# Performance work log

Hardware: AMD Instinct MI355X
Metric: run time of the kernel (lower is better)

Reference implementation:

```python
import jax, jax.numpy as jnp
import numpy as np

N, D, M, E, K = 16384, 512, 1024, 8, 2
LOSS_COEF = 0.01
EPS = 1e-10


def setup_inputs() -> dict:
    key = jax.random.key(0)
    ks = jax.random.split(key, 6)
    x = jax.random.normal(ks[0], (N, D), dtype=jnp.float32)
    # gate weight (torch init is zeros; use small random so routing is non-degenerate)
    w_gate = 0.02 * jax.random.normal(ks[1], (D, E), dtype=jnp.float32)
    # stacked expert FFN params: Linear(D->M), GELU, Linear(M->D)
    W1 = jax.random.normal(ks[2], (E, D, M), dtype=jnp.float32) / np.sqrt(D)
    b1 = jnp.zeros((E, M), dtype=jnp.float32)
    W2 = jax.random.normal(ks[3], (E, M, D), dtype=jnp.float32) / np.sqrt(M)
    b2 = jnp.zeros((E, D), dtype=jnp.float32)
    return {"x": x, "w_gate": w_gate, "W1": W1, "b1": b1, "W2": W2, "b2": b2}


def _cv_squared(v):
    # torch .var() is unbiased (ddof=1)
    v = v.astype(jnp.float32)
    return jnp.var(v, ddof=1) / (jnp.mean(v) ** 2 + EPS)


def reference(x, w_gate, W1, b1, W2, b2):
    n = x.shape[0]
    # --- noisy_top_k_gating (eval path: no noise) ---
    logits = x @ w_gate                                  # [N, E]
    top_logits, top_idx = jax.lax.top_k(logits, min(K + 1, E))
    topk_logits = top_logits[:, :K]                      # [N, K]
    topk_idx = top_idx[:, :K]                            # [N, K]
    topk_gates = jax.nn.softmax(topk_logits, axis=-1)    # [N, K]
    gates = jnp.zeros_like(logits).at[jnp.arange(n)[:, None], topk_idx].set(topk_gates)
    importance = gates.sum(axis=0)                       # [E]
    load = (gates > 0).sum(axis=0).astype(jnp.float32)   # [E]
    loss = LOSS_COEF * (_cv_squared(importance) + _cv_squared(load))
    # --- experts (dense equivalent of sparse dispatch/combine: gate==0 rows contribute 0) ---
    h = jnp.einsum('nd,edm->enm', x, W1) + b1[:, None, :]     # [E, N, M]
    h = jax.nn.gelu(h, approximate=False)
    out = jnp.einsum('enm,emd->end', h, W2) + b2[:, None, :]  # [E, N, D]
    y = jnp.einsum('ne,end->nd', gates, out)                  # [N, D]
    return (y, loss)
```

## Files before the change

### kernel.cpp

```cpp
#include <hip/hip_runtime.h>
#include <math.h>

#define NTOK 16384
#define DDIM 512
#define MDIM 1024
#define NEXP 8
#define BKW 32
#define TMAX 264

typedef __attribute__((ext_vector_type(8))) short short8;
typedef __attribute__((ext_vector_type(4))) float floatx4;

__device__ inline unsigned short f2bf(float f){
  union { float f; unsigned int u; } v; v.f = f;
  unsigned int u = v.u;
  u += ((u >> 16) & 1u) + 0x7fffu;
  return (unsigned short)(u >> 16);
}

__device__ inline float bf2f(unsigned short s){
  union { unsigned int u; float f; } v;
  v.u = ((unsigned int)s) << 16;
  return v.f;
}

__device__ inline float gelu_fast(float x){
  float u = x * 0.70710678118654752f;
  float a = fabsf(u);
  float t = __builtin_amdgcn_rcpf(fmaf(0.3275911f, a, 1.0f));
  float p = fmaf(1.061405429f, t, -1.453152027f);
  p = fmaf(p, t, 1.421413741f);
  p = fmaf(p, t, -0.284496736f);
  p = fmaf(p, t, 0.254829592f);
  p = p * t;
  float e = __expf(-u * u);
  float erfa = fmaf(-p, e, 1.0f);
  float erfu = copysignf(erfa, u);
  return 0.5f * x * (1.0f + erfu);
}

__device__ __forceinline__ void gload16(const unsigned short* g, unsigned short* l){
  __builtin_amdgcn_global_load_lds(
      (const __attribute__((address_space(1))) void*)g,
      (__attribute__((address_space(3))) void*)l,
      16, 0, 0);
}


__global__ __launch_bounds__(256)
void prep_gating_kernel(const float* __restrict__ x,
                        const float* __restrict__ wg,
                        const float* __restrict__ W1, const float* __restrict__ W2,
                        unsigned short* __restrict__ xb,
                        unsigned short* __restrict__ w1t, unsigned short* __restrict__ w2t,
                        int* __restrict__ tok_e, float* __restrict__ tok_g,
                        int* __restrict__ counts, float* __restrict__ imp){
  __shared__ float tile[32][33];
  __shared__ int   lcnt[NEXP];
  __shared__ float limp[NEXP];
  int t = threadIdx.x;

  if (blockIdx.x >= 1024){
    int pb = blockIdx.x - 1024;
    int bx = pb & 31, by = (pb >> 5) & 15, z = pb >> 9;
    const float* in; unsigned short* out; int R, C, c0, r0, e;
    if (z < 8){ e = z;     in = W1; out = w1t; R = DDIM; C = MDIM; c0 = bx << 5; r0 = by << 5; }
    else      { e = z - 8; in = W2; out = w2t; R = MDIM; C = DDIM; c0 = by << 5; r0 = bx << 5; }
    const float* src = in + (size_t)e * R * C;
    unsigned short* dst = out + (size_t)e * R * C;
    int tc = t & 31;
    int tr = t >> 5;
    #pragma unroll
    for (int i = 0; i < 32; i += 8)
      tile[tr + i][tc] = src[(size_t)(r0 + tr + i) * C + c0 + tc];
    __syncthreads();
    #pragma unroll
    for (int i = 0; i < 32; i += 8)
      dst[(size_t)(c0 + tr + i) * R + r0 + tc] = f2bf(tile[tc][tr + i]);
    return;
  }

  if (t < NEXP){ lcnt[t] = 0; limp[t] = 0.0f; }
  __syncthreads();

  int wave = t >> 6;
  int lane = t & 63;

  for (int it = 0; it < 4; it++){
    int n = blockIdx.x * 16 + it * 4 + wave;

    const float4* xp = (const float4*)(x + (size_t)n * DDIM + lane * 8);
    float4 a = xp[0], b = xp[1];
    float xv[8] = {a.x, a.y, a.z, a.w, b.x, b.y, b.z, b.w};

    short8 xo;
    #pragma unroll
    for (int j = 0; j < 8; j++) xo[j] = (short)f2bf(xv[j]);
    *(short8*)(xb + (size_t)n * DDIM + lane * 8) = xo;

    double acc[NEXP];
    #pragma unroll
    for (int e = 0; e < NEXP; e++) acc[e] = 0.0;
    #pragma unroll
    for (int j = 0; j < 8; j++){
      const float* wr = wg + (size_t)(lane * 8 + j) * NEXP;
      #pragma unroll
      for (int e = 0; e < NEXP; e++) acc[e] += (double)xv[j] * (double)wr[e];
    }
    #pragma unroll
    for (int off = 32; off >= 1; off >>= 1){
      #pragma unroll
      for (int e = 0; e < NEXP; e++) acc[e] += __shfl_xor(acc[e], off);
    }
    if (lane == 0){
      int i0 = -1, i1 = -1;
      double l0 = -1e300, l1 = -1e300;
      #pragma unroll
      for (int e = 0; e < NEXP; e++){
        double v = acc[e];
        if (v > l0){ l1 = l0; i1 = i0; l0 = v; i0 = e; }
        else if (v > l1){ l1 = v; i1 = e; }
      }
      float ex = expf((float)(l1 - l0));
      float g0 = 1.0f / (1.0f + ex);
      float g1 = ex / (1.0f + ex);
      tok_e[n * 2]     = i0; tok_e[n * 2 + 1] = i1;
      tok_g[n * 2]     = g0; tok_g[n * 2 + 1] = g1;
      atomicAdd(&lcnt[i0], 1); atomicAdd(&lcnt[i1], 1);
      atomicAdd(&limp[i0], g0); atomicAdd(&limp[i1], g1);
    }
  }
  __syncthreads();
  if (t < NEXP){
    atomicAdd(&counts[t], lcnt[t]);
    atomicAdd(&imp[t], limp[t]);
  }
}


__global__ __launch_bounds__(256)
void scatter_kernel(const int* __restrict__ counts,
                    const float* __restrict__ imp,
                    const int* __restrict__ tok_e,
                    int* __restrict__ rank,
                    int* __restrict__ offsets_g, int* __restrict__ tile_pre_g,
                    int* __restrict__ btok, int* __restrict__ slot_tok2,
                    float* __restrict__ out_loss){
  __shared__ int lcnt[NEXP];
  __shared__ int lbase[NEXP];
  int t = threadIdx.x;
  if (t < NEXP) lcnt[t] = 0;
  __syncthreads();

  int n = blockIdx.x * 256 + t;
  int e0 = tok_e[n * 2], e1 = tok_e[n * 2 + 1];
  int r0 = atomicAdd(&lcnt[e0], 1);
  int r1 = atomicAdd(&lcnt[e1], 1);
  __syncthreads();
  if (t < NEXP){
    int offacc = 0;
    #pragma unroll
    for (int e = 0; e < NEXP; e++){ int c = counts[e]; if (e < t) offacc += c; }
    lbase[t] = offacc + atomicAdd(&rank[t], lcnt[t]);
  }
  __syncthreads();
  int s0 = lbase[e0] + r0;
  int s1 = lbase[e1] + r1;
  btok[s0] = n;
  btok[s1] = n;
  slot_tok2[s0] = n * 2;
  slot_tok2[s1] = n * 2 + 1;

  if (blockIdx.x == 0 && t < 64){
    int l = t;
    int   c  = (l < NEXP) ? counts[l] : 0;
    float im = (l < NEXP) ? imp[l]    : 0.0f;
    int   tl = (c + 127) >> 7;
    int poff = 0, ptl = 0, tot = 0, tott = 0;
    double si = 0, si2 = 0, sl = 0, sl2 = 0;
    #pragma unroll
    for (int e = 0; e < NEXP; e++){
      int   ce = __shfl(c, e);
      int   te = __shfl(tl, e);
      float ie = __shfl(im, e);
      if (e < l){ poff += ce; ptl += te; }
      tot += ce; tott += te;
      si += (double)ie; si2 += (double)ie * ie;
      sl += (double)ce; sl2 += (double)ce * ce;
    }
    if (l < NEXP){ offsets_g[l] = poff; tile_pre_g[l] = ptl; }
    if (l == 0){
      offsets_g[NEXP] = tot; tile_pre_g[NEXP] = tott;
      double mi = si / 8.0, ml = sl / 8.0;
      double vi = (si2 - 8.0 * mi * mi) / 7.0;
      double vl = (sl2 - 8.0 * ml * ml) / 7.0;
      *out_loss = (float)(0.01 * (vi / (mi * mi + 1e-10) + vl / (ml * ml + 1e-10)));
    }
  }
}


__global__ __launch_bounds__(512, 6)
void gemm1_kernel(const unsigned short* __restrict__ xb,
                  const unsigned short* __restrict__ w1t,
                  const float* __restrict__ b1,
                  const int* __restrict__ offsets,
                  const int* __restrict__ tile_pre,
                  const int* __restrict__ btok,
                  unsigned short* __restrict__ H){
  int b = blockIdx.x;
  int L = (b & 7) * TMAX + (b >> 3);
  int ct = L & 7;
  int tt = L >> 3;
  if (tt >= tile_pre[NEXP]) return;
  int e = 0;
  while (tt >= tile_pre[e + 1]) e++;
  int rt = tt - tile_pre[e];
  int off = offsets[e];
  int cnt = offsets[e + 1] - off;
  int r0 = rt << 7;

  __shared__ unsigned short As[3 * 128 * BKW];
  __shared__ unsigned short Bs[3 * 128 * BKW];

  int t = threadIdx.x;
  int w = t >> 6;
  int l = t & 63;
  int g = (l & 3) ^ ((l >> 3) & 3);

  const unsigned short* apt;
  {
    int ra = r0 + w * 16 + (l >> 2);  if (ra >= cnt) ra = cnt - 1;
    apt = xb + (size_t)btok[off + ra] * DDIM + g * 8;
  }
  const unsigned short* bpt = w1t + ((size_t)e * MDIM + (ct << 7) + w * 16 + (l >> 2)) * DDIM + g * 8;

  int wr = (w >> 1) << 5;
  int wc = (w & 1) << 6;
  int lm = l & 15;
  int lq = l >> 4;
  int swz = (lm >> 1) & 3;

  int aoff[2], boff[4];
  #pragma unroll
  for (int i = 0; i < 2; i++) aoff[i] = (wr + i * 16 + lm) * BKW + ((lq ^ swz) << 3);
  #pragma unroll
  for (int j = 0; j < 4; j++) boff[j] = (wc + j * 16 + lm) * BKW + ((lq ^ swz) << 3);

  floatx4 acc[2][4] = {};

  #define STAGE1(K0, CB) {                                   \
    gload16(apt + (K0), As + (CB) * 4096 + w * 512);         \
    gload16(bpt + (K0), Bs + (CB) * 4096 + w * 512);         \
  }
  #define READ1(CB) {                                        \
    const unsigned short* Ac = As + (CB) * 4096;             \
    const unsigned short* Bc = Bs + (CB) * 4096;             \
    _Pragma("unroll")                                        \
    for (int i = 0; i < 2; i++) af[i]  = *(const short8*)(Ac + aoff[i]); \
    _Pragma("unroll")                                        \
    for (int j = 0; j < 4; j++) bfr[j] = *(const short8*)(Bc + boff[j]); \
  }
  #define MFMA1 {                                            \
    _Pragma("unroll")                                        \
    for (int i = 0; i < 2; i++)                              \
      _Pragma("unroll")                                      \
      for (int j = 0; j < 4; j++)                            \
        acc[i][j] = __builtin_amdgcn_mfma_f32_16x16x32_bf16(af[i], bfr[j], acc[i][j], 0, 0, 0); \
  }
  #define WAITBAR(N) {                                       \
    asm volatile("s_waitcnt vmcnt(" #N ")" ::: "memory");    \
    __builtin_amdgcn_sched_barrier(0);                       \
    __builtin_amdgcn_s_barrier();                            \
    __builtin_amdgcn_sched_barrier(0);                       \
  }

  const int NK = DDIM / BKW;
  STAGE1(0, 0);
  STAGE1(BKW, 1);
  WAITBAR(2);
  #pragma unroll
  for (int k = 0; k < NK; k++){
    const int cur = k % 3;
    short8 af[2], bfr[4];
    READ1(cur);
    if (k < NK - 2) STAGE1((k + 2) * BKW, (k + 2) % 3);
    __builtin_amdgcn_s_setprio(1);
    MFMA1;
    __builtin_amdgcn_s_setprio(0);
    if (k < NK - 2){ WAITBAR(2); }
    else if (k == NK - 2){ WAITBAR(0); }
  }
  #undef STAGE1
  #undef READ1
  #undef MFMA1
  #undef WAITBAR

  const float* bias = b1 + e * MDIM + (ct << 7);
  #pragma unroll
  for (int i = 0; i < 2; i++){
    int rbase = wr + i * 16 + lq * 4;
    #pragma unroll
    for (int j = 0; j < 4; j++){
      int cc = wc + j * 16 + lm;
      float bv = bias[cc];
      #pragma unroll
      for (int r = 0; r < 4; r++){
        int row = r0 + rbase + r;
        if (row < cnt){
          float v = acc[i][j][r] + bv;
          H[(size_t)(off + row) * MDIM + (ct << 7) + cc] = f2bf(gelu_fast(v));
        }
      }
    }
  }
}

__global__ __launch_bounds__(512, 6)
void gemm2_kernel(const unsigned short* __restrict__ H,
                  const unsigned short* __restrict__ w2t,
                  const float* __restrict__ b2,
                  const int* __restrict__ offsets,
                  const int* __restrict__ tile_pre,
                  const int* __restrict__ slot_tok2,
                  unsigned short* __restrict__ O){
  int b = blockIdx.x;
  int L = (b & 7) * (TMAX / 2) + (b >> 3);
  int ct = L & 3;
  int tt = L >> 2;
  if (tt >= tile_pre[NEXP]) return;
  int e = 0;
  while (tt >= tile_pre[e + 1]) e++;
  int rt = tt - tile_pre[e];
  int off = offsets[e];
  int cnt = offsets[e + 1] - off;
  int r0 = rt << 7;

  __shared__ unsigned short As[3 * 128 * BKW];
  __shared__ unsigned short Bs[3 * 128 * BKW];

  int t = threadIdx.x;
  int w = t >> 6;
  int l = t & 63;
  int g = (l & 3) ^ ((l >> 3) & 3);

  const unsigned short* apt;
  {
    int ra = r0 + w * 16 + (l >> 2);  if (ra >= cnt) ra = cnt - 1;
    apt = H + (size_t)(off + ra) * MDIM + g * 8;
  }
  const unsigned short* bpt = w2t + ((size_t)e * DDIM + (ct << 7) + w * 16 + (l >> 2)) * MDIM + g * 8;

  int wr = (w >> 1) << 5;
  int wc = (w & 1) << 6;
  int lm = l & 15;
  int lq = l >> 4;
  int swz = (lm >> 1) & 3;

  int aoff[2], boff[4];
  #pragma unroll
  for (int i = 0; i < 2; i++) aoff[i] = (wr + i * 16 + lm) * BKW + ((lq ^ swz) << 3);
  #pragma unroll
  for (int j = 0; j < 4; j++) boff[j] = (wc + j * 16 + lm) * BKW + ((lq ^ swz) << 3);

  floatx4 acc[2][4] = {};

  #define STAGE2(K0, CB) {                                   \
    gload16(apt + (K0), As + (CB) * 4096 + w * 512);         \
    gload16(bpt + (K0), Bs + (CB) * 4096 + w * 512);         \
  }
  #define READ2(CB) {                                        \
    const unsigned short* Ac = As + (CB) * 4096;             \
    const unsigned short* Bc = Bs + (CB) * 4096;             \
    _Pragma("unroll")                                        \
    for (int i = 0; i < 2; i++) af[i]  = *(const short8*)(Ac + aoff[i]); \
    _Pragma("unroll")                                        \
    for (int j = 0; j < 4; j++) bfr[j] = *(const short8*)(Bc + boff[j]); \
  }
  #define MFMA2 {                                            \
    _Pragma("unroll")                                        \
    for (int i = 0; i < 2; i++)                              \
      _Pragma("unroll")                                      \
      for (int j = 0; j < 4; j++)                            \
        acc[i][j] = __builtin_amdgcn_mfma_f32_16x16x32_bf16(af[i], bfr[j], acc[i][j], 0, 0, 0); \
  }
  #define WAITBAR2(N) {                                      \
    asm volatile("s_waitcnt vmcnt(" #N ")" ::: "memory");    \
    __builtin_amdgcn_sched_barrier(0);                       \
    __builtin_amdgcn_s_barrier();                            \
    __builtin_amdgcn_sched_barrier(0);                       \
  }

  const int NK = MDIM / BKW;
  STAGE2(0, 0);
  STAGE2(BKW, 1);
  WAITBAR2(2);
  #pragma unroll
  for (int k = 0; k < NK; k++){
    const int cur = k % 3;
    short8 af[2], bfr[4];
    READ2(cur);
    if (k < NK - 2) STAGE2((k + 2) * BKW, (k + 2) % 3);
    __builtin_amdgcn_s_setprio(1);
    MFMA2;
    __builtin_amdgcn_s_setprio(0);
    if (k < NK - 2){ WAITBAR2(2); }
    else if (k == NK - 2){ WAITBAR2(0); }
  }
  #undef STAGE2
  #undef READ2
  #undef MFMA2
  #undef WAITBAR2

  const float* bias = b2 + e * DDIM + (ct << 7);
  #pragma unroll
  for (int i = 0; i < 2; i++){
    int rbase = wr + i * 16 + lq * 4;
    #pragma unroll
    for (int r = 0; r < 4; r++){
      int row = r0 + rbase + r;
      if (row < cnt){
        int t2 = slot_tok2[off + row];
        #pragma unroll
        for (int j = 0; j < 4; j++){
          int cc = wc + j * 16 + lm;
          O[(size_t)t2 * DDIM + (ct << 7) + cc] = f2bf(acc[i][j][r] + bias[cc]);
        }
      }
    }
  }
}


__global__ __launch_bounds__(256)
void combine_kernel(const unsigned short* __restrict__ O,
                    const float* __restrict__ tok_g,
                    float* __restrict__ y){
  int wave = threadIdx.x >> 6;
  int lane = threadIdx.x & 63;
  int n = blockIdx.x * 4 + wave;
  float g0 = tok_g[n * 2], g1 = tok_g[n * 2 + 1];
  short8 a = *(const short8*)(O + (size_t)(n * 2)     * DDIM + lane * 8);
  short8 b = *(const short8*)(O + (size_t)(n * 2 + 1) * DDIM + lane * 8);
  float4 o0, o1;
  float* po0 = (float*)&o0;
  float* po1 = (float*)&o1;
  #pragma unroll
  for (int j = 0; j < 4; j++){
    po0[j] = g0 * bf2f((unsigned short)a[j]) + g1 * bf2f((unsigned short)b[j]);
    po1[j] = g0 * bf2f((unsigned short)a[j + 4]) + g1 * bf2f((unsigned short)b[j + 4]);
  }
  float4* yp = (float4*)(y + (size_t)n * DDIM + lane * 8);
  yp[0] = o0;
  yp[1] = o1;
}


extern "C" void kernel_launch(void* const* d_in, const int* in_sizes, int n_in,
                              void* d_out, int out_size, void* d_ws, size_t ws_size,
                              hipStream_t stream){
  const float* x  = (const float*)d_in[0];
  const float* wg = (const float*)d_in[1];
  const float* W1 = (const float*)d_in[2];
  const float* b1 = (const float*)d_in[3];
  const float* W2 = (const float*)d_in[4];
  const float* b2 = (const float*)d_in[5];
  float* y = (float*)d_out;

  char* ws = (char*)d_ws;
  size_t o = 0;
  auto alloc = [&](size_t bytes)->char*{
    char* p = ws + o;
    o += (bytes + 255) & ~(size_t)255;
    return p;
  };
  unsigned short* xb   = (unsigned short*)alloc((size_t)NTOK * DDIM * 2);
  unsigned short* w1t  = (unsigned short*)alloc((size_t)NEXP * MDIM * DDIM * 2);
  unsigned short* w2t  = (unsigned short*)alloc((size_t)NEXP * DDIM * MDIM * 2);
  unsigned short* H    = (unsigned short*)alloc((size_t)NTOK * 2 * MDIM * 2);
  unsigned short* O    = (unsigned short*)alloc((size_t)NTOK * 2 * DDIM * 2);
  int*   btok     = (int*)  alloc((size_t)NTOK * 2 * 4);
  int*   slot_tok2= (int*)  alloc((size_t)NTOK * 2 * 4);
  int*   tok_e    = (int*)  alloc((size_t)NTOK * 2 * 4);
  float* tok_g    = (float*)alloc((size_t)NTOK * 2 * 4);
  int*   counts   = (int*)  alloc(64);
  float* imp      = (float*)alloc(64);
  int*   rank     = (int*)  alloc(64);
  int*   offsets  = (int*)  alloc(64);
  int*   tile_pre = (int*)  alloc(64);

  hipMemsetAsync(counts, 0, 768, stream);
  hipLaunchKernelGGL(prep_gating_kernel, dim3(1024 + 8192), dim3(256), 0, stream,
                     x, wg, W1, W2, xb, w1t, w2t, tok_e, tok_g, counts, imp);
  hipLaunchKernelGGL(scatter_kernel, dim3(NTOK / 256), dim3(256), 0, stream,
                     counts, imp, tok_e, rank, offsets, tile_pre,
                     btok, slot_tok2, y + (size_t)NTOK * DDIM);
  hipLaunchKernelGGL(gemm1_kernel, dim3(TMAX * 8), dim3(512), 0, stream,
                     xb, w1t, b1, offsets, tile_pre, btok, H);
  hipLaunchKernelGGL(gemm2_kernel, dim3(TMAX * 4), dim3(512), 0, stream,
                     H, w2t, b2, offsets, tile_pre, slot_tok2, O);
  hipLaunchKernelGGL(combine_kernel, dim3(NTOK / 4), dim3(256), 0, stream,
                     O, tok_g, y);
}
```

Before: 271.5 us.

## Split GEMM k-step into two MFMA phases and separate weight prep kernel

In both expert GEMM kernels, each k-step now reads half the B fragments, runs half the MFMAs, hits a workgroup barrier, then reads the other half and runs the rest, with explicit lgkmcnt waits. The goal is to interleave LDS reads with MFMA work and keep waves in step. This adds an extra barrier and forced LDS waits on every iteration. Separately, the fused prep/gating kernel is split into a weight transpose/convert kernel that also zeroes the counters, which removes the memset call but adds one more kernel launch.

```diff
diff --git a/kernel.cpp b/kernel.cpp
--- a/kernel.cpp
+++ b/kernel.cpp
@@ -47,39 +47,42 @@
 }
 
 
+__global__ void prep_kernel(const float* __restrict__ W1, const float* __restrict__ W2,
+                            unsigned short* __restrict__ w1t, unsigned short* __restrict__ w2t,
+                            int* __restrict__ counts, float* __restrict__ imp,
+                            int* __restrict__ rank){
+  __shared__ float tile[32][33];
+  int z = blockIdx.z;
+  if (z == 0 && blockIdx.x == 0 && blockIdx.y == 0){
+    int flat = threadIdx.y * 32 + threadIdx.x;
+    if (flat < NEXP){ counts[flat] = 0; imp[flat] = 0.0f; rank[flat] = 0; }
+  }
+  const float* in; unsigned short* out; int R, C, c0, r0, e;
+  if (z < 8){ e = z;     in = W1; out = w1t; R = DDIM; C = MDIM; c0 = blockIdx.x << 5; r0 = blockIdx.y << 5; }
+  else      { e = z - 8; in = W2; out = w2t; R = MDIM; C = DDIM; c0 = blockIdx.y << 5; r0 = blockIdx.x << 5; }
+  const float* src = in + (size_t)e * R * C;
+  unsigned short* dst = out + (size_t)e * R * C;
+  int tc = threadIdx.x;
+  int tr = threadIdx.y;
+  #pragma unroll
+  for (int i = 0; i < 32; i += 8)
+    tile[tr + i][tc] = src[(size_t)(r0 + tr + i) * C + c0 + tc];
+  __syncthreads();
+  #pragma unroll
+  for (int i = 0; i < 32; i += 8)
+    dst[(size_t)(c0 + tr + i) * R + r0 + tc] = f2bf(tile[tc][tr + i]);
+}
+
+
 __global__ __launch_bounds__(256)
-void prep_gating_kernel(const float* __restrict__ x,
-                        const float* __restrict__ wg,
-                        const float* __restrict__ W1, const float* __restrict__ W2,
-                        unsigned short* __restrict__ xb,
-                        unsigned short* __restrict__ w1t, unsigned short* __restrict__ w2t,
-                        int* __restrict__ tok_e, float* __restrict__ tok_g,
-                        int* __restrict__ counts, float* __restrict__ imp){
-  __shared__ float tile[32][33];
+void gating_kernel(const float* __restrict__ x,
+                   const float* __restrict__ wg,
+                   unsigned short* __restrict__ xb,
+                   int* __restrict__ tok_e, float* __restrict__ tok_g,
+                   int* __restrict__ counts, float* __restrict__ imp){
   __shared__ int   lcnt[NEXP];
   __shared__ float limp[NEXP];
   int t = threadIdx.x;
-
-  if (blockIdx.x >= 1024){
-    int pb = blockIdx.x - 1024;
-    int bx = pb & 31, by = (pb >> 5) & 15, z = pb >> 9;
-    const float* in; unsigned short* out; int R, C, c0, r0, e;
-    if (z < 8){ e = z;     in = W1; out = w1t; R = DDIM; C = MDIM; c0 = bx << 5; r0 = by << 5; }
-    else      { e = z - 8; in = W2; out = w2t; R = MDIM; C = DDIM; c0 = by << 5; r0 = bx << 5; }
-    const float* src = in + (size_t)e * R * C;
-    unsigned short* dst = out + (size_t)e * R * C;
-    int tc = t & 31;
-    int tr = t >> 5;
-    #pragma unroll
-    for (int i = 0; i < 32; i += 8)
-      tile[tr + i][tc] = src[(size_t)(r0 + tr + i) * C + c0 + tc];
-    __syncthreads();
-    #pragma unroll
-    for (int i = 0; i < 32; i += 8)
-      dst[(size_t)(c0 + tr + i) * R + r0 + tc] = f2bf(tile[tc][tr + i]);
-    return;
-  }
-
   if (t < NEXP){ lcnt[t] = 0; limp[t] = 0.0f; }
   __syncthreads();
 
@@ -253,20 +256,36 @@
     gload16(apt + (K0), As + (CB) * 4096 + w * 512);         \
     gload16(bpt + (K0), Bs + (CB) * 4096 + w * 512);         \
   }
-  #define READ1(CB) {                                        \
+  #define READA1(CB) {                                       \
     const unsigned short* Ac = As + (CB) * 4096;             \
     const unsigned short* Bc = Bs + (CB) * 4096;             \
-    _Pragma("unroll")                                        \
-    for (int i = 0; i < 2; i++) af[i]  = *(const short8*)(Ac + aoff[i]); \
-    _Pragma("unroll")                                        \
-    for (int j = 0; j < 4; j++) bfr[j] = *(const short8*)(Bc + boff[j]); \
-  }
-  #define MFMA1 {                                            \
+    af[0]  = *(const short8*)(Ac + aoff[0]);                 \
+    af[1]  = *(const short8*)(Ac + aoff[1]);                 \
+    bfr[0] = *(const short8*)(Bc + boff[0]);                 \
+    bfr[1] = *(const short8*)(Bc + boff[1]);                 \
+  }
+  #define READB1(CB) {                                       \
+    const unsigned short* Bc = Bs + (CB) * 4096;             \
+    bfr[2] = *(const short8*)(Bc + boff[2]);                 \
+    bfr[3] = *(const short8*)(Bc + boff[3]);                 \
+  }
+  #define MFMA_A1 {                                          \
     _Pragma("unroll")                                        \
     for (int i = 0; i < 2; i++)                              \
       _Pragma("unroll")                                      \
-      for (int j = 0; j < 4; j++)                            \
+      for (int j = 0; j < 2; j++)                            \
         acc[i][j] = __builtin_amdgcn_mfma_f32_16x16x32_bf16(af[i], bfr[j], acc[i][j], 0, 0, 0); \
+  }
+  #define MFMA_B1 {                                          \
+    _Pragma("unroll")                                        \
+    for (int i = 0; i < 2; i++)                              \
+      _Pragma("unroll")                                      \
+      for (int j = 2; j < 4; j++)                            \
+        acc[i][j] = __builtin_amdgcn_mfma_f32_16x16x32_bf16(af[i], bfr[j], acc[i][j], 0, 0, 0); \
+  }
+  #define LGKM0 {                                            \
+    asm volatile("s_waitcnt lgkmcnt(0)" ::: "memory");       \
+    __builtin_amdgcn_sched_barrier(0);                       \
   }
   #define WAITBAR(N) {                                       \
     asm volatile("s_waitcnt vmcnt(" #N ")" ::: "memory");    \
@@ -283,17 +302,27 @@
   for (int k = 0; k < NK; k++){
     const int cur = k % 3;
     short8 af[2], bfr[4];
-    READ1(cur);
+    READA1(cur);
     if (k < NK - 2) STAGE1((k + 2) * BKW, (k + 2) % 3);
+    LGKM0;
     __builtin_amdgcn_s_setprio(1);
-    MFMA1;
+    MFMA_A1;
+    __builtin_amdgcn_s_setprio(0);
+    __builtin_amdgcn_s_barrier();
+    READB1(cur);
+    LGKM0;
+    __builtin_amdgcn_s_setprio(1);
+    MFMA_B1;
     __builtin_amdgcn_s_setprio(0);
     if (k < NK - 2){ WAITBAR(2); }
     else if (k == NK - 2){ WAITBAR(0); }
   }
   #undef STAGE1
-  #undef READ1
-  #undef MFMA1
+  #undef READA1
+  #undef READB1
+  #undef MFMA_A1
+  #undef MFMA_B1
+  #undef LGKM0
   #undef WAITBAR
 
   const float* bias = b1 + e * MDIM + (ct << 7);
@@ -369,20 +398,36 @@
     gload16(apt + (K0), As + (CB) * 4096 + w * 512);         \
     gload16(bpt + (K0), Bs + (CB) * 4096 + w * 512);         \
   }
-  #define READ2(CB) {                                        \
+  #define READA2(CB) {                                       \
     const unsigned short* Ac = As + (CB) * 4096;             \
     const unsigned short* Bc = Bs + (CB) * 4096;             \
-    _Pragma("unroll")                                        \
-    for (int i = 0; i < 2; i++) af[i]  = *(const short8*)(Ac + aoff[i]); \
-    _Pragma("unroll")                                        \
-    for (int j = 0; j < 4; j++) bfr[j] = *(const short8*)(Bc + boff[j]); \
-  }
-  #define MFMA2 {                                            \
+    af[0]  = *(const short8*)(Ac + aoff[0]);                 \
+    af[1]  = *(const short8*)(Ac + aoff[1]);                 \
+    bfr[0] = *(const short8*)(Bc + boff[0]);                 \
+    bfr[1] = *(const short8*)(Bc + boff[1]);                 \
+  }
+  #define READB2(CB) {                                       \
+    const unsigned short* Bc = Bs + (CB) * 4096;             \
+    bfr[2] = *(const short8*)(Bc + boff[2]);                 \
+    bfr[3] = *(const short8*)(Bc + boff[3]);                 \
+  }
+  #define MFMA_A2 {                                          \
     _Pragma("unroll")                                        \
     for (int i = 0; i < 2; i++)                              \
       _Pragma("unroll")                                      \
-      for (int j = 0; j < 4; j++)                            \
+      for (int j = 0; j < 2; j++)                            \
         acc[i][j] = __builtin_amdgcn_mfma_f32_16x16x32_bf16(af[i], bfr[j], acc[i][j], 0, 0, 0); \
+  }
+  #define MFMA_B2 {                                          \
+    _Pragma("unroll")                                        \
+    for (int i = 0; i < 2; i++)                              \
+      _Pragma("unroll")                                      \
+      for (int j = 2; j < 4; j++)                            \
+        acc[i][j] = __builtin_amdgcn_mfma_f32_16x16x32_bf16(af[i], bfr[j], acc[i][j], 0, 0, 0); \
+  }
+  #define LGKM0 {                                            \
+    asm volatile("s_waitcnt lgkmcnt(0)" ::: "memory");       \
+    __builtin_amdgcn_sched_barrier(0);                       \
   }
   #define WAITBAR2(N) {                                      \
     asm volatile("s_waitcnt vmcnt(" #N ")" ::: "memory");    \
@@ -399,17 +444,27 @@
   for (int k = 0; k < NK; k++){
     const int cur = k % 3;
     short8 af[2], bfr[4];
-    READ2(cur);
+    READA2(cur);
     if (k < NK - 2) STAGE2((k + 2) * BKW, (k + 2) % 3);
+    LGKM0;
     __builtin_amdgcn_s_setprio(1);
-    MFMA2;
+    MFMA_A2;
+    __builtin_amdgcn_s_setprio(0);
+    __builtin_amdgcn_s_barrier();
+    READB2(cur);
+    LGKM0;
+    __builtin_amdgcn_s_setprio(1);
+    MFMA_B2;
     __builtin_amdgcn_s_setprio(0);
     if (k < NK - 2){ WAITBAR2(2); }
     else if (k == NK - 2){ WAITBAR2(0); }
   }
   #undef STAGE2
-  #undef READ2
-  #undef MFMA2
+  #undef READA2
+  #undef READB2
+  #undef MFMA_A2
+  #undef MFMA_B2
+  #undef LGKM0
   #undef WAITBAR2
 
   const float* bias = b2 + e * DDIM + (ct << 7);
@@ -489,9 +544,10 @@
   int*   offsets  = (int*)  alloc(64);
   int*   tile_pre = (int*)  alloc(64);
 
-  hipMemsetAsync(counts, 0, 768, stream);
-  hipLaunchKernelGGL(prep_gating_kernel, dim3(1024 + 8192), dim3(256), 0, stream,
-                     x, wg, W1, W2, xb, w1t, w2t, tok_e, tok_g, counts, imp);
+  hipLaunchKernelGGL(prep_kernel, dim3(32, 16, 16), dim3(32, 8), 0, stream,
+                     W1, W2, w1t, w2t, counts, imp, rank);
+  hipLaunchKernelGGL(gating_kernel, dim3(NTOK / 16), dim3(256), 0, stream,
+                     x, wg, xb, tok_e, tok_g, counts, imp);
   hipLaunchKernelGGL(scatter_kernel, dim3(NTOK / 256), dim3(256), 0, stream,
                      counts, imp, tok_e, rank, offsets, tile_pre,
                      btok, slot_tok2, y + (size_t)NTOK * DDIM);
```

After: 268.5 us. About the same (-1.1%).

## Use double-buffered GEMM pipelines and split weight prep from gating

Applied to the files above, without the earlier changes.

Both expert GEMM kernels drop from a three-stage LDS ring to two buffers. Each iteration now issues the next stage's loads before reading the current buffer, then waits with vmcnt(0) and a barrier. This halves LDS use per block, which may allow more blocks per CU, but it leaves less global-load latency hidden behind MFMA work. Separately, the fused weight-transpose and gating kernel is split into a separate transpose kernel and a gating kernel. The transpose kernel also zeroes the counters, which removes the memset call at the cost of one extra kernel launch.

```diff
diff --git a/kernel.cpp b/kernel.cpp
--- a/kernel.cpp
+++ b/kernel.cpp
@@ -47,39 +47,42 @@
 }
 
 
+__global__ void prep_kernel(const float* __restrict__ W1, const float* __restrict__ W2,
+                            unsigned short* __restrict__ w1t, unsigned short* __restrict__ w2t,
+                            int* __restrict__ counts, float* __restrict__ imp,
+                            int* __restrict__ rank){
+  __shared__ float tile[32][33];
+  int z = blockIdx.z;
+  if (z == 0 && blockIdx.x == 0 && blockIdx.y == 0){
+    int flat = threadIdx.y * 32 + threadIdx.x;
+    if (flat < NEXP){ counts[flat] = 0; imp[flat] = 0.0f; rank[flat] = 0; }
+  }
+  const float* in; unsigned short* out; int R, C, c0, r0, e;
+  if (z < 8){ e = z;     in = W1; out = w1t; R = DDIM; C = MDIM; c0 = blockIdx.x << 5; r0 = blockIdx.y << 5; }
+  else      { e = z - 8; in = W2; out = w2t; R = MDIM; C = DDIM; c0 = blockIdx.y << 5; r0 = blockIdx.x << 5; }
+  const float* src = in + (size_t)e * R * C;
+  unsigned short* dst = out + (size_t)e * R * C;
+  int tc = threadIdx.x;
+  int tr = threadIdx.y;
+  #pragma unroll
+  for (int i = 0; i < 32; i += 8)
+    tile[tr + i][tc] = src[(size_t)(r0 + tr + i) * C + c0 + tc];
+  __syncthreads();
+  #pragma unroll
+  for (int i = 0; i < 32; i += 8)
+    dst[(size_t)(c0 + tr + i) * R + r0 + tc] = f2bf(tile[tc][tr + i]);
+}
+
+
 __global__ __launch_bounds__(256)
-void prep_gating_kernel(const float* __restrict__ x,
-                        const float* __restrict__ wg,
-                        const float* __restrict__ W1, const float* __restrict__ W2,
-                        unsigned short* __restrict__ xb,
-                        unsigned short* __restrict__ w1t, unsigned short* __restrict__ w2t,
-                        int* __restrict__ tok_e, float* __restrict__ tok_g,
-                        int* __restrict__ counts, float* __restrict__ imp){
-  __shared__ float tile[32][33];
+void gating_kernel(const float* __restrict__ x,
+                   const float* __restrict__ wg,
+                   unsigned short* __restrict__ xb,
+                   int* __restrict__ tok_e, float* __restrict__ tok_g,
+                   int* __restrict__ counts, float* __restrict__ imp){
   __shared__ int   lcnt[NEXP];
   __shared__ float limp[NEXP];
   int t = threadIdx.x;
-
-  if (blockIdx.x >= 1024){
-    int pb = blockIdx.x - 1024;
-    int bx = pb & 31, by = (pb >> 5) & 15, z = pb >> 9;
-    const float* in; unsigned short* out; int R, C, c0, r0, e;
-    if (z < 8){ e = z;     in = W1; out = w1t; R = DDIM; C = MDIM; c0 = bx << 5; r0 = by << 5; }
-    else      { e = z - 8; in = W2; out = w2t; R = MDIM; C = DDIM; c0 = by << 5; r0 = bx << 5; }
-    const float* src = in + (size_t)e * R * C;
-    unsigned short* dst = out + (size_t)e * R * C;
-    int tc = t & 31;
-    int tr = t >> 5;
-    #pragma unroll
-    for (int i = 0; i < 32; i += 8)
-      tile[tr + i][tc] = src[(size_t)(r0 + tr + i) * C + c0 + tc];
-    __syncthreads();
-    #pragma unroll
-    for (int i = 0; i < 32; i += 8)
-      dst[(size_t)(c0 + tr + i) * R + r0 + tc] = f2bf(tile[tc][tr + i]);
-    return;
-  }
-
   if (t < NEXP){ lcnt[t] = 0; limp[t] = 0.0f; }
   __syncthreads();
 
@@ -220,8 +223,8 @@
   int cnt = offsets[e + 1] - off;
   int r0 = rt << 7;
 
-  __shared__ unsigned short As[3 * 128 * BKW];
-  __shared__ unsigned short Bs[3 * 128 * BKW];
+  __shared__ unsigned short As[2 * 128 * BKW];
+  __shared__ unsigned short Bs[2 * 128 * BKW];
 
   int t = threadIdx.x;
   int w = t >> 6;
@@ -268,8 +271,8 @@
       for (int j = 0; j < 4; j++)                            \
         acc[i][j] = __builtin_amdgcn_mfma_f32_16x16x32_bf16(af[i], bfr[j], acc[i][j], 0, 0, 0); \
   }
-  #define WAITBAR(N) {                                       \
-    asm volatile("s_waitcnt vmcnt(" #N ")" ::: "memory");    \
+  #define WAITBAR {                                          \
+    asm volatile("s_waitcnt vmcnt(0)" ::: "memory");         \
     __builtin_amdgcn_sched_barrier(0);                       \
     __builtin_amdgcn_s_barrier();                            \
     __builtin_amdgcn_sched_barrier(0);                       \
@@ -277,19 +280,16 @@
 
   const int NK = DDIM / BKW;
   STAGE1(0, 0);
-  STAGE1(BKW, 1);
-  WAITBAR(2);
+  WAITBAR;
   #pragma unroll
   for (int k = 0; k < NK; k++){
-    const int cur = k % 3;
     short8 af[2], bfr[4];
-    READ1(cur);
-    if (k < NK - 2) STAGE1((k + 2) * BKW, (k + 2) % 3);
+    if (k + 1 < NK) STAGE1((k + 1) * BKW, (k + 1) & 1);
+    READ1(k & 1);
     __builtin_amdgcn_s_setprio(1);
     MFMA1;
     __builtin_amdgcn_s_setprio(0);
-    if (k < NK - 2){ WAITBAR(2); }
-    else if (k == NK - 2){ WAITBAR(0); }
+    if (k + 1 < NK){ WAITBAR; }
   }
   #undef STAGE1
   #undef READ1
@@ -336,8 +336,8 @@
   int cnt = offsets[e + 1] - off;
   int r0 = rt << 7;
 
-  __shared__ unsigned short As[3 * 128 * BKW];
-  __shared__ unsigned short Bs[3 * 128 * BKW];
+  __shared__ unsigned short As[2 * 128 * BKW];
+  __shared__ unsigned short Bs[2 * 128 * BKW];
 
   int t = threadIdx.x;
   int w = t >> 6;
@@ -384,8 +384,8 @@
       for (int j = 0; j < 4; j++)                            \
         acc[i][j] = __builtin_amdgcn_mfma_f32_16x16x32_bf16(af[i], bfr[j], acc[i][j], 0, 0, 0); \
   }
-  #define WAITBAR2(N) {                                      \
-    asm volatile("s_waitcnt vmcnt(" #N ")" ::: "memory");    \
+  #define WAITBAR2 {                                         \
+    asm volatile("s_waitcnt vmcnt(0)" ::: "memory");         \
     __builtin_amdgcn_sched_barrier(0);                       \
     __builtin_amdgcn_s_barrier();                            \
     __builtin_amdgcn_sched_barrier(0);                       \
@@ -393,19 +393,16 @@
 
   const int NK = MDIM / BKW;
   STAGE2(0, 0);
-  STAGE2(BKW, 1);
-  WAITBAR2(2);
+  WAITBAR2;
   #pragma unroll
   for (int k = 0; k < NK; k++){
-    const int cur = k % 3;
     short8 af[2], bfr[4];
-    READ2(cur);
-    if (k < NK - 2) STAGE2((k + 2) * BKW, (k + 2) % 3);
+    if (k + 1 < NK) STAGE2((k + 1) * BKW, (k + 1) & 1);
+    READ2(k & 1);
     __builtin_amdgcn_s_setprio(1);
     MFMA2;
     __builtin_amdgcn_s_setprio(0);
-    if (k < NK - 2){ WAITBAR2(2); }
-    else if (k == NK - 2){ WAITBAR2(0); }
+    if (k + 1 < NK){ WAITBAR2; }
   }
   #undef STAGE2
   #undef READ2
@@ -489,9 +486,10 @@
   int*   offsets  = (int*)  alloc(64);
   int*   tile_pre = (int*)  alloc(64);
 
-  hipMemsetAsync(counts, 0, 768, stream);
-  hipLaunchKernelGGL(prep_gating_kernel, dim3(1024 + 8192), dim3(256), 0, stream,
-                     x, wg, W1, W2, xb, w1t, w2t, tok_e, tok_g, counts, imp);
+  hipLaunchKernelGGL(prep_kernel, dim3(32, 16, 16), dim3(32, 8), 0, stream,
+                     W1, W2, w1t, w2t, counts, imp, rank);
+  hipLaunchKernelGGL(gating_kernel, dim3(NTOK / 16), dim3(256), 0, stream,
+                     x, wg, xb, tok_e, tok_g, counts, imp);
   hipLaunchKernelGGL(scatter_kernel, dim3(NTOK / 256), dim3(256), 0, stream,
                      counts, imp, tok_e, rank, offsets, tile_pre,
                      btok, slot_tok2, y + (size_t)NTOK * DDIM);
```

Measured after the change: 270.1 us. About the same (-0.5%).
